# Performance work log

Hardware: AMD Instinct MI355X
Metric: run time of the kernel (lower is better)

## Reference

```python
import jax, jax.numpy as jnp
import numpy as np

NUM_ROWS = 4096      # out_features
GROUP_COUNT = 32
GROUP_SIZE = 128     # in_features = GROUP_COUNT * GROUP_SIZE = 4096
CODEBOOK_SIZE = 16   # 4-bit codes


def setup_inputs() -> dict:
    key = jax.random.key(0)
    k1, k2, k3, k4 = jax.random.split(key, 4)
    x = jax.random.normal(k1, (2, 1024, GROUP_COUNT * GROUP_SIZE), dtype=jnp.float32)
    codebooks = jax.random.normal(k2, (NUM_ROWS, GROUP_COUNT, CODEBOOK_SIZE), dtype=jnp.float32)
    codes = jax.random.randint(k3, (NUM_ROWS, GROUP_COUNT, GROUP_SIZE), 0, CODEBOOK_SIZE, dtype=jnp.int32)
    bias = jax.random.normal(k4, (NUM_ROWS,), dtype=jnp.float32)
    return {"x": x, "codebooks": codebooks, "codes": codes, "bias": bias}


def _dequantize_weight(codes, codebooks):
    # codes: [R, G, S] int indices into last dim of codebooks [R, G, B]
    R, G, S = codes.shape
    W_hat = jnp.take_along_axis(codebooks, codes, axis=2)  # [R, G, S]
    return W_hat.reshape(R, G * S)  # [out_features, in_features]


def reference(x, codebooks, codes, bias):
    W = _dequantize_weight(codes, codebooks)           # [out, in]
    out = jnp.einsum("bsi,oi->bso", x, W) + bias       # F.linear
    return out
```

## Files before the change

kernel.cpp:

```cpp
#include <hip/hip_runtime.h>
#include <hip/hip_bf16.h>
#include <stdint.h>


#define M_DIM 2048
#define N_DIM 4096
#define K_DIM 4096

typedef __attribute__((ext_vector_type(4))) int i32x4;

__device__ __forceinline__ uint32_t pack4(int a, int b, int c, int d) {
    return (uint32_t)(a & 255) | ((uint32_t)(b & 255) << 8) |
           ((uint32_t)(c & 255) << 16) | ((uint32_t)(d & 255) << 24);
}

__device__ __forceinline__ int q8(float v, float inv) {
    return (int)rintf(v * inv);
}

__global__ __launch_bounds__(256) void prepass_q8(
    const float* __restrict__ cb,
    const int* __restrict__ codes,
    const float* __restrict__ x,
    uint4* __restrict__ wq,
    uint4* __restrict__ xq,
    float* __restrict__ sw,
    float* __restrict__ sx)
{
    __shared__ float scb[512];
    __shared__ float red[256];
    const int b = blockIdx.x, t = threadIdx.x;
    const int c  = t;
    const int kt = c >> 3, wkc = (c >> 2) & 1, qd = c & 3;
    if (b < N_DIM) {
        const int o = b;
        const float c0 = cb[(size_t)o * 512 + t];
        const float c1 = cb[(size_t)o * 512 + 256 + t];
        scb[t] = c0; scb[t + 256] = c1;
        red[t] = fmaxf(fabsf(c0), fabsf(c1));
        __syncthreads();
        for (int s = 128; s > 0; s >>= 1) {
            if (t < s) red[t] = fmaxf(red[t], red[t + s]);
            __syncthreads();
        }
        const float amax = fmaxf(red[0], 1e-20f);
        const float inv = 127.0f / amax;
        if (t == 0) sw[o] = amax / 127.0f;
        const int4* crow = (const int4*)(codes + (size_t)o * K_DIM);
        const int4 i0 = crow[c * 4 + 0];
        const int4 i1 = crow[c * 4 + 1];
        const int4 i2 = crow[c * 4 + 2];
        const int4 i3 = crow[c * 4 + 3];
        const float* g = scb + (c >> 3) * 16;
        uint4 ov;
        ov.x = pack4(q8(g[i0.x], inv), q8(g[i0.y], inv), q8(g[i0.z], inv), q8(g[i0.w], inv));
        ov.y = pack4(q8(g[i1.x], inv), q8(g[i1.y], inv), q8(g[i1.z], inv), q8(g[i1.w], inv));
        ov.z = pack4(q8(g[i2.x], inv), q8(g[i2.y], inv), q8(g[i2.z], inv), q8(g[i2.w], inv));
        ov.w = pack4(q8(g[i3.x], inv), q8(g[i3.y], inv), q8(g[i3.z], inv), q8(g[i3.w], inv));
        const int nt = o >> 7, wn2 = (o >> 6) & 1, ir = (o >> 4) & 3, l15 = o & 15;
        const size_t idx = ((size_t)(nt * 32 + kt) * 16 + (wn2 * 2 + wkc) * 4 + ir) * 64
                           + qd * 16 + l15;
        wq[idx] = ov;
    } else {
        const int m = b - N_DIM;
        const float4* row = (const float4*)(x + (size_t)m * K_DIM);
        float4 v[4];
        float am = 0.f;
#pragma unroll
        for (int j = 0; j < 4; ++j) {
            v[j] = row[c * 4 + j];
            am = fmaxf(am, fmaxf(fmaxf(fabsf(v[j].x), fabsf(v[j].y)),
                                 fmaxf(fabsf(v[j].z), fabsf(v[j].w))));
        }
        red[t] = am;
        __syncthreads();
        for (int s = 128; s > 0; s >>= 1) {
            if (t < s) red[t] = fmaxf(red[t], red[t + s]);
            __syncthreads();
        }
        const float amax = fmaxf(red[0], 1e-20f);
        const float inv = 127.0f / amax;
        if (t == 0) sx[m] = amax / 127.0f;
        uint4 ov;
        ov.x = pack4(q8(v[0].x, inv), q8(v[0].y, inv), q8(v[0].z, inv), q8(v[0].w, inv));
        ov.y = pack4(q8(v[1].x, inv), q8(v[1].y, inv), q8(v[1].z, inv), q8(v[1].w, inv));
        ov.z = pack4(q8(v[2].x, inv), q8(v[2].y, inv), q8(v[2].z, inv), q8(v[2].w, inv));
        ov.w = pack4(q8(v[3].x, inv), q8(v[3].y, inv), q8(v[3].z, inv), q8(v[3].w, inv));
        const int mt = m >> 8, wm2 = (m >> 7) & 1, ir = (m >> 4) & 7, l15 = m & 15;
        const size_t idx = ((size_t)(mt * 32 + kt) * 32 + (wm2 * 2 + wkc) * 8 + ir) * 64
                           + qd * 16 + l15;
        xq[idx] = ov;
    }
}


__device__ __forceinline__ void load_frags(
    const i32x4* __restrict__ pA, const i32x4* __restrict__ pB,
    int kt, i32x4 a[8], i32x4 b[4])
{
#pragma unroll
    for (int i = 0; i < 8; ++i) a[i] = pA[(size_t)kt * 2048 + i * 64];
#pragma unroll
    for (int i = 0; i < 4; ++i) b[i] = pB[(size_t)kt * 1024 + i * 64];
}

__device__ __forceinline__ void mfma_tile(
    const i32x4 a[8], const i32x4 b[4], i32x4 acc[8][4])
{
#pragma unroll
    for (int mi = 0; mi < 8; ++mi)
#pragma unroll
        for (int ni = 0; ni < 4; ++ni)
            acc[mi][ni] = __builtin_amdgcn_mfma_i32_16x16x64_i8(
                a[mi], b[ni], acc[mi][ni], 0, 0, 0);
}

__global__ __launch_bounds__(512, 2) void gemm_i8(
    const i32x4* __restrict__ A,
    const i32x4* __restrict__ B,
    const float* __restrict__ sx,
    const float* __restrict__ sw,
    const float* __restrict__ bias,
    float* __restrict__ C)
{
    __shared__ __align__(16) unsigned char smem[65536];

    const int tid  = threadIdx.x;
    const int w    = tid >> 6;
    const int lane = tid & 63;
    const int l15  = lane & 15;
    const int quad = lane >> 4;
    const int nt   = blockIdx.x;
    const int mt   = blockIdx.y;
    const int m0   = mt * 256;
    const int n0   = nt * 128;
    const int wk   = w >> 2;
    const int wm2  = (w >> 1) & 1;
    const int wn2  = w & 1;
    const int wm   = wm2 * 128;
    const int wn   = wn2 * 64;

    const i32x4* pA = A + (size_t)mt * 65536 + (size_t)(wm2 * 2 + wk) * 512 + lane;
    const i32x4* pB = B + (size_t)nt * 32768 + (size_t)(wn2 * 2 + wk) * 256 + lane;

    i32x4 acc[8][4] = {};
    i32x4 aA[8], bA[4], aB[8], bB[4];

    load_frags(pA, pB, 0, aA, bA);
    for (int kt = 0; kt < 30; kt += 2) {
        load_frags(pA, pB, kt + 1, aB, bB);
        mfma_tile(aA, bA, acc);
        load_frags(pA, pB, kt + 2, aA, bA);
        mfma_tile(aB, bB, acc);
    }
    load_frags(pA, pB, 31, aB, bB);
    mfma_tile(aA, bA, acc);
    mfma_tile(aB, bB, acc);

    i32x4* red = (i32x4*)smem;
    if (w == 4 || w == 5) {
        i32x4* dst = red + (w & 1) * 2048;
#pragma unroll
        for (int mi = 0; mi < 8; ++mi)
#pragma unroll
            for (int ni = 0; ni < 4; ++ni)
                dst[(mi * 4 + ni) * 64 + lane] = acc[mi][ni];
    }
    __syncthreads();
    if (w == 0 || w == 1) {
        const i32x4* src = red + (w & 1) * 2048;
#pragma unroll
        for (int mi = 0; mi < 8; ++mi)
#pragma unroll
            for (int ni = 0; ni < 4; ++ni) {
                const i32x4 v = src[(mi * 4 + ni) * 64 + lane];
                acc[mi][ni] = acc[mi][ni] + v;
            }
    }
    __syncthreads();
    if (w == 6 || w == 7) {
        i32x4* dst = red + (w & 1) * 2048;
#pragma unroll
        for (int mi = 0; mi < 8; ++mi)
#pragma unroll
            for (int ni = 0; ni < 4; ++ni)
                dst[(mi * 4 + ni) * 64 + lane] = acc[mi][ni];
    }
    __syncthreads();
    if (w == 2 || w == 3) {
        const i32x4* src = red + (w & 1) * 2048;
#pragma unroll
        for (int mi = 0; mi < 8; ++mi)
#pragma unroll
            for (int ni = 0; ni < 4; ++ni) {
                const i32x4 v = src[(mi * 4 + ni) * 64 + lane];
                acc[mi][ni] = acc[mi][ni] + v;
            }
    }

    if (w < 4) {
        float swv[4], bv[4];
#pragma unroll
        for (int ni = 0; ni < 4; ++ni) {
            const int col = n0 + wn + ni * 16 + l15;
            swv[ni] = sw[col];
            bv[ni]  = bias[col];
        }
#pragma unroll
        for (int mi = 0; mi < 8; ++mi) {
            float sxr[4];
#pragma unroll
            for (int r = 0; r < 4; ++r)
                sxr[r] = sx[m0 + wm + mi * 16 + quad * 4 + r];
#pragma unroll
            for (int ni = 0; ni < 4; ++ni) {
                const int col = n0 + wn + ni * 16 + l15;
                float* cp = C + (size_t)(m0 + wm + mi * 16 + quad * 4) * N_DIM + col;
#pragma unroll
                for (int r = 0; r < 4; ++r)
                    cp[(size_t)r * N_DIM] =
                        (float)acc[mi][ni][r] * (sxr[r] * swv[ni]) + bv[ni];
            }
        }
    }
}

__global__ __launch_bounds__(256) void naive_kernel(
    const float* __restrict__ x, const float* __restrict__ cb,
    const int* __restrict__ codes, const float* __restrict__ bias,
    float* __restrict__ out)
{
    const size_t idx = (size_t)blockIdx.x * 256 + threadIdx.x;
    const int n = (int)(idx & 4095);
    const int m = (int)(idx >> 12);
    const float* xr = x + (size_t)m * K_DIM;
    float s = bias[n];
    for (int g = 0; g < 32; ++g) {
        const float* cbr = cb + ((size_t)n * 32 + g) * 16;
        const int* cr = codes + ((size_t)n * 32 + g) * 128;
        const float* xg = xr + g * 128;
        for (int ss = 0; ss < 128; ++ss) s += xg[ss] * cbr[cr[ss]];
    }
    out[idx] = s;
}

extern "C" void kernel_launch(void* const* d_in, const int* in_sizes, int n_in,
                              void* d_out, int out_size, void* d_ws, size_t ws_size,
                              hipStream_t stream) {
    const float* x     = (const float*)d_in[0];
    const float* cb    = (const float*)d_in[1];
    const int*   codes = (const int*)d_in[2];
    const float* bias  = (const float*)d_in[3];
    float* out = (float*)d_out;

    const size_t szW = (size_t)N_DIM * K_DIM;
    const size_t szX = (size_t)M_DIM * K_DIM;
    const size_t need = szW + szX + (N_DIM + M_DIM) * sizeof(float);

    if (ws_size >= need) {
        unsigned char* Wq = (unsigned char*)d_ws;
        unsigned char* Xq = Wq + szW;
        float* sw = (float*)(Xq + szX);
        float* sx = sw + N_DIM;
        prepass_q8<<<dim3(N_DIM + M_DIM), dim3(256), 0, stream>>>(
            cb, codes, x, (uint4*)Wq, (uint4*)Xq, sw, sx);
        gemm_i8<<<dim3(N_DIM / 128, M_DIM / 256), dim3(512), 0, stream>>>(
            (const i32x4*)Xq, (const i32x4*)Wq, sx, sw, bias, out);
    } else {
        naive_kernel<<<dim3((M_DIM * N_DIM) / 256), dim3(256), 0, stream>>>(x, cb, codes, bias, out);
    }
}
```

Before: 195.5 us.

## Split quantization prepass into scale and coalesced-write quantize kernels

Separates per-row scale computation into its own kernel, then runs a quantize kernel whose blocks cover 16 rows so each wavefront writes a contiguous run of packed int8 fragments in the GEMM layout. This targets the scattered, poorly coalesced stores of the old single-pass prepass. In exchange, x and the codebooks are read twice and an extra kernel launch is added.

```diff
diff --git a/kernel.cpp b/kernel.cpp
--- a/kernel.cpp
+++ b/kernel.cpp
@@ -18,78 +18,108 @@
     return (int)rintf(v * inv);
 }
 
-__global__ __launch_bounds__(256) void prepass_q8(
+__global__ __launch_bounds__(256) void scales_k(
     const float* __restrict__ cb,
-    const int* __restrict__ codes,
     const float* __restrict__ x,
-    uint4* __restrict__ wq,
-    uint4* __restrict__ xq,
-    float* __restrict__ sw,
-    float* __restrict__ sx)
-{
-    __shared__ float scb[512];
+    float* __restrict__ sw, float* __restrict__ swInv,
+    float* __restrict__ sx, float* __restrict__ sxInv)
+{
     __shared__ float red[256];
     const int b = blockIdx.x, t = threadIdx.x;
-    const int c  = t;
-    const int kt = c >> 3, wkc = (c >> 2) & 1, qd = c & 3;
     if (b < N_DIM) {
         const int o = b;
         const float c0 = cb[(size_t)o * 512 + t];
         const float c1 = cb[(size_t)o * 512 + 256 + t];
-        scb[t] = c0; scb[t + 256] = c1;
         red[t] = fmaxf(fabsf(c0), fabsf(c1));
         __syncthreads();
         for (int s = 128; s > 0; s >>= 1) {
             if (t < s) red[t] = fmaxf(red[t], red[t + s]);
             __syncthreads();
         }
-        const float amax = fmaxf(red[0], 1e-20f);
-        const float inv = 127.0f / amax;
-        if (t == 0) sw[o] = amax / 127.0f;
-        const int4* crow = (const int4*)(codes + (size_t)o * K_DIM);
-        const int4 i0 = crow[c * 4 + 0];
-        const int4 i1 = crow[c * 4 + 1];
-        const int4 i2 = crow[c * 4 + 2];
-        const int4 i3 = crow[c * 4 + 3];
-        const float* g = scb + (c >> 3) * 16;
+        if (t == 0) {
+            const float amax = fmaxf(red[0], 1e-20f);
+            sw[o] = amax / 127.0f;
+            swInv[o] = 127.0f / amax;
+        }
+    } else {
+        const int m = b - N_DIM;
+        const float* row = x + (size_t)m * K_DIM;
+        float am = 0.f;
+#pragma unroll
+        for (int i = 0; i < 4; ++i) {
+            const float4 v = *(const float4*)(row + (size_t)(t + i * 256) * 4);
+            am = fmaxf(am, fmaxf(fmaxf(fabsf(v.x), fabsf(v.y)),
+                                 fmaxf(fabsf(v.z), fabsf(v.w))));
+        }
+        red[t] = am;
+        __syncthreads();
+        for (int s = 128; s > 0; s >>= 1) {
+            if (t < s) red[t] = fmaxf(red[t], red[t + s]);
+            __syncthreads();
+        }
+        if (t == 0) {
+            const float amax = fmaxf(red[0], 1e-20f);
+            sx[m] = amax / 127.0f;
+            sxInv[m] = 127.0f / amax;
+        }
+    }
+}
+
+__global__ __launch_bounds__(256) void quant_k(
+    const float* __restrict__ cb,
+    const int* __restrict__ codes,
+    const float* __restrict__ x,
+    const float* __restrict__ swInv,
+    const float* __restrict__ sxInv,
+    uint4* __restrict__ wq,
+    uint4* __restrict__ xq)
+{
+    const int b = blockIdx.x, t = threadIdx.x;
+    const int w = t >> 6, lane = t & 63;
+    const int l15 = lane & 15, qd = lane >> 4;
+    if (b < 4096) {
+        __shared__ float scb[16 * 36];
+        const int o0 = (b >> 4) * 16, pq = b & 15;
+        const int p = pq * 4 + w;
+        const int ktp = p >> 1, wkc = p & 1;
+        const int g0 = pq * 2;
+#pragma unroll
+        for (int u = 0; u < 2; ++u) {
+            const int e = t + u * 256;
+            const int r = e >> 5, gg = (e >> 4) & 1, j = e & 15;
+            scb[r * 36 + gg * 18 + j] = cb[(size_t)(o0 + r) * 512 + (g0 + gg) * 16 + j];
+        }
+        __syncthreads();
+        const float inv = swInv[o0 + l15];
+        const int c = ktp * 8 + wkc * 4 + qd;
+        const int4* cr = (const int4*)codes + (size_t)(o0 + l15) * 1024 + c * 4;
+        const int4 i0 = cr[0], i1 = cr[1], i2 = cr[2], i3 = cr[3];
+        const float* g = scb + l15 * 36 + (w >> 1) * 18;
         uint4 ov;
         ov.x = pack4(q8(g[i0.x], inv), q8(g[i0.y], inv), q8(g[i0.z], inv), q8(g[i0.w], inv));
         ov.y = pack4(q8(g[i1.x], inv), q8(g[i1.y], inv), q8(g[i1.z], inv), q8(g[i1.w], inv));
         ov.z = pack4(q8(g[i2.x], inv), q8(g[i2.y], inv), q8(g[i2.z], inv), q8(g[i2.w], inv));
         ov.w = pack4(q8(g[i3.x], inv), q8(g[i3.y], inv), q8(g[i3.z], inv), q8(g[i3.w], inv));
-        const int nt = o >> 7, wn2 = (o >> 6) & 1, ir = (o >> 4) & 3, l15 = o & 15;
-        const size_t idx = ((size_t)(nt * 32 + kt) * 16 + (wn2 * 2 + wkc) * 4 + ir) * 64
-                           + qd * 16 + l15;
-        wq[idx] = ov;
+        const int nt = o0 >> 7, wn2 = (o0 >> 6) & 1, ir = (o0 >> 4) & 3;
+        const size_t base = ((size_t)(nt * 32 + ktp) * 16 + (wn2 * 2 + wkc) * 4 + ir) * 64;
+        wq[base + lane] = ov;
     } else {
-        const int m = b - N_DIM;
-        const float4* row = (const float4*)(x + (size_t)m * K_DIM);
-        float4 v[4];
-        float am = 0.f;
-#pragma unroll
-        for (int j = 0; j < 4; ++j) {
-            v[j] = row[c * 4 + j];
-            am = fmaxf(am, fmaxf(fmaxf(fabsf(v[j].x), fabsf(v[j].y)),
-                                 fmaxf(fabsf(v[j].z), fabsf(v[j].w))));
-        }
-        red[t] = am;
-        __syncthreads();
-        for (int s = 128; s > 0; s >>= 1) {
-            if (t < s) red[t] = fmaxf(red[t], red[t + s]);
-            __syncthreads();
-        }
-        const float amax = fmaxf(red[0], 1e-20f);
-        const float inv = 127.0f / amax;
-        if (t == 0) sx[m] = amax / 127.0f;
+        const int bb = b - 4096;
+        const int m0 = (bb >> 4) * 16, pq = bb & 15;
+        const int p = pq * 4 + w;
+        const int ktp = p >> 1, wkc = p & 1;
+        const float inv = sxInv[m0 + l15];
+        const int c = ktp * 8 + wkc * 4 + qd;
+        const float4* xr = (const float4*)x + (size_t)(m0 + l15) * 1024 + c * 4;
+        const float4 v0 = xr[0], v1 = xr[1], v2 = xr[2], v3 = xr[3];
         uint4 ov;
-        ov.x = pack4(q8(v[0].x, inv), q8(v[0].y, inv), q8(v[0].z, inv), q8(v[0].w, inv));
-        ov.y = pack4(q8(v[1].x, inv), q8(v[1].y, inv), q8(v[1].z, inv), q8(v[1].w, inv));
-        ov.z = pack4(q8(v[2].x, inv), q8(v[2].y, inv), q8(v[2].z, inv), q8(v[2].w, inv));
-        ov.w = pack4(q8(v[3].x, inv), q8(v[3].y, inv), q8(v[3].z, inv), q8(v[3].w, inv));
-        const int mt = m >> 8, wm2 = (m >> 7) & 1, ir = (m >> 4) & 7, l15 = m & 15;
-        const size_t idx = ((size_t)(mt * 32 + kt) * 32 + (wm2 * 2 + wkc) * 8 + ir) * 64
-                           + qd * 16 + l15;
-        xq[idx] = ov;
+        ov.x = pack4(q8(v0.x, inv), q8(v0.y, inv), q8(v0.z, inv), q8(v0.w, inv));
+        ov.y = pack4(q8(v1.x, inv), q8(v1.y, inv), q8(v1.z, inv), q8(v1.w, inv));
+        ov.z = pack4(q8(v2.x, inv), q8(v2.y, inv), q8(v2.z, inv), q8(v2.w, inv));
+        ov.w = pack4(q8(v3.x, inv), q8(v3.y, inv), q8(v3.z, inv), q8(v3.w, inv));
+        const int mt = m0 >> 8, wm2 = (m0 >> 7) & 1, ir = (m0 >> 4) & 7;
+        const size_t base = ((size_t)(mt * 32 + ktp) * 32 + (wm2 * 2 + wkc) * 8 + ir) * 64;
+        xq[base + lane] = ov;
     }
 }
 
@@ -255,15 +285,19 @@
 
     const size_t szW = (size_t)N_DIM * K_DIM;
     const size_t szX = (size_t)M_DIM * K_DIM;
-    const size_t need = szW + szX + (N_DIM + M_DIM) * sizeof(float);
+    const size_t need = szW + szX + 2 * (N_DIM + M_DIM) * sizeof(float);
 
     if (ws_size >= need) {
         unsigned char* Wq = (unsigned char*)d_ws;
         unsigned char* Xq = Wq + szW;
-        float* sw = (float*)(Xq + szX);
-        float* sx = sw + N_DIM;
-        prepass_q8<<<dim3(N_DIM + M_DIM), dim3(256), 0, stream>>>(
-            cb, codes, x, (uint4*)Wq, (uint4*)Xq, sw, sx);
+        float* sw    = (float*)(Xq + szX);
+        float* sx    = sw + N_DIM;
+        float* swInv = sx + M_DIM;
+        float* sxInv = swInv + N_DIM;
+        scales_k<<<dim3(N_DIM + M_DIM), dim3(256), 0, stream>>>(
+            cb, x, sw, swInv, sx, sxInv);
+        quant_k<<<dim3(4096 + 2048), dim3(256), 0, stream>>>(
+            cb, codes, x, swInv, sxInv, (uint4*)Wq, (uint4*)Xq);
         gemm_i8<<<dim3(N_DIM / 128, M_DIM / 256), dim3(512), 0, stream>>>(
             (const i32x4*)Xq, (const i32x4*)Wq, sx, sw, bias, out);
     } else {
```

Result: faster. 187.3 us (-4.2%).
